# Kernel tuning notes

Measured on AMD Instinct MI355X. Metric: run time of the kernel, lower is better.

Reference implementation:

```python
import jax, jax.numpy as jnp
import numpy as np

N_HEADS = 4

def setup_inputs() -> dict:
    key = jax.random.key(0)
    B, S, D = 4, 2048, 256
    ks = jax.random.split(key, 9)
    sd = 1.0 / np.sqrt(D)
    return {
        "x":  jax.random.normal(ks[0], (B, S, D), jnp.float32),
        "Wq": jax.random.normal(ks[1], (D, D), jnp.float32) * sd,
        "bq": jax.random.normal(ks[2], (D,), jnp.float32) * 0.02,
        "Wk": jax.random.normal(ks[3], (D, D), jnp.float32) * sd,
        "bk": jax.random.normal(ks[4], (D,), jnp.float32) * 0.02,
        "Wv": jax.random.normal(ks[5], (D, D), jnp.float32) * sd,
        "bv": jax.random.normal(ks[6], (D,), jnp.float32) * 0.02,
        "Wo": jax.random.normal(ks[7], (D, D), jnp.float32) * sd,
        "bo": jax.random.normal(ks[8], (D,), jnp.float32) * 0.02,
    }

def reference(x, Wq, bq, Wk, bk, Wv, bv, Wo, bo):
    B, S, D = x.shape
    H = N_HEADS
    W = D // H
    # QKV projections, split heads: (B,S,D) -> (B,H,S,W)
    def heads(t):
        return t.reshape(B, S, H, W).transpose(0, 2, 1, 3)
    q = heads(x @ Wq + bq)
    k = heads(x @ Wk + bk)
    v = heads(x @ Wv + bv)
    scores = jnp.einsum('bhqw,bhkw->bhqk', q, k) / jnp.sqrt(jnp.float32(W))
    # multiplicative distance-decay mask: mask[i,j] = (S - |i-j|)/S
    i = jnp.arange(S, dtype=jnp.float32)
    mask = (S - jnp.abs(i[:, None] - i[None, :])) / S  # (S,S)
    scores = jax.nn.softmax(scores * mask, axis=-1)
    h = jnp.einsum('bhqk,bhkw->bhqw', scores, v)
    h = h.transpose(0, 2, 1, 3).reshape(B, S, D)  # merge heads
    return h @ Wo + bo
```

## Files before the change

### kernel.cpp

```cpp
#include <hip/hip_runtime.h>
#include <hip/hip_bf16.h>

#define S_LEN 2048
#define DMODEL 256
#define NH 4
#define HDIM 64

typedef __attribute__((ext_vector_type(8))) short short8;
typedef __attribute__((ext_vector_type(4))) float floatx4;
typedef __hip_bfloat16 bf16;

__device__ __forceinline__ floatx4 mfma16(short8 a, short8 b, floatx4 c) {
    return __builtin_amdgcn_mfma_f32_16x16x32_bf16(a, b, c, 0, 0, 0);
}
__device__ __forceinline__ void gload16(const void* gp, void* lp) {
    __builtin_amdgcn_global_load_lds(
        (const __attribute__((address_space(1))) void*)gp,
        (__attribute__((address_space(3))) void*)lp, 16, 0, 0);
}
__device__ __forceinline__ unsigned cvtpk(float lo, float hi) {
    unsigned r;
    asm("v_cvt_pk_bf16_f32 %0, %1, %2" : "=v"(r) : "v"(lo), "v"(hi));
    return r;
}
__device__ __forceinline__ void p32swap(int &a, int &b) {
    auto res = __builtin_amdgcn_permlane32_swap((unsigned)a, (unsigned)b, false, false);
    a = (int)res[0]; b = (int)res[1];
}
#if __has_builtin(__builtin_amdgcn_permlane16_swap)
#define HAVE_P16 1
__device__ __forceinline__ void p16swap(int &a, int &b) {
    auto res = __builtin_amdgcn_permlane16_swap((unsigned)a, (unsigned)b, false, false);
    a = (int)res[0]; b = (int)res[1];
}
#else
#define HAVE_P16 0
#endif
__device__ __forceinline__ float ex2(float x) {
#if __has_builtin(__builtin_amdgcn_exp2f)
    return __builtin_amdgcn_exp2f(x);
#else
    return __expf(x * 0.6931471805599453f);
#endif
}

__global__ __launch_bounds__(256) void prep_kernel(
    const float* __restrict__ x,
    const float* __restrict__ Wq, const float* __restrict__ Wk,
    const float* __restrict__ Wv, const float* __restrict__ Wo,
    bf16* __restrict__ xb, bf16* __restrict__ wtq, bf16* __restrict__ wtk,
    bf16* __restrict__ wtv, bf16* __restrict__ wto)
{
    __shared__ bf16 sT[64 * 72];
    const int t = threadIdx.x;
    const int blk = blockIdx.x;
    if (blk < 256) {
        int base = blk * 8192 + t * 8;
#pragma unroll
        for (int j = 0; j < 4; ++j) {
            int idx = base + j * 2048;
            float4 f0 = *(const float4*)&x[idx];
            float4 f1 = *(const float4*)&x[idx + 4];
            union { bf16 h[8]; short8 v; } o;
            o.h[0] = __float2bfloat16(f0.x); o.h[1] = __float2bfloat16(f0.y);
            o.h[2] = __float2bfloat16(f0.z); o.h[3] = __float2bfloat16(f0.w);
            o.h[4] = __float2bfloat16(f1.x); o.h[5] = __float2bfloat16(f1.y);
            o.h[6] = __float2bfloat16(f1.z); o.h[7] = __float2bfloat16(f1.w);
            *(short8*)&xb[idx] = o.v;
        }
    } else {
        int blk2 = blk - 256;
        int wi = blk2 >> 2;
        int n0 = (blk2 & 3) * 64;
        const float* ws = (wi == 0) ? Wq : (wi == 1) ? Wk : (wi == 2) ? Wv : Wo;
        bf16* wd = (wi == 0) ? wtq : (wi == 1) ? wtk : (wi == 2) ? wtv : wto;
        for (int k0 = 0; k0 < 256; k0 += 64) {
            __syncthreads();
#pragma unroll
            for (int j = 0; j < 16; ++j) {
                int idx = j * 256 + t;
                int kk = idx >> 6, nn = idx & 63;
                sT[nn * 72 + kk] = __float2bfloat16(ws[(k0 + kk) * 256 + n0 + nn]);
            }
            __syncthreads();
#pragma unroll
            for (int j2 = 0; j2 < 2; ++j2) {
                int c = j2 * 256 + t;
                int nn = c >> 3, seg = c & 7;
                *(short8*)&wd[(n0 + nn) * 256 + k0 + seg * 8] = *(const short8*)&sT[nn * 72 + seg * 8];
            }
        }
    }
}

__global__ __launch_bounds__(256) void proj_kernel(
    const bf16* __restrict__ xb, const bf16* __restrict__ hb,
    const bf16* __restrict__ wtq, const bf16* __restrict__ wtk,
    const bf16* __restrict__ wtv, const bf16* __restrict__ wto,
    const float* __restrict__ bq, const float* __restrict__ bk,
    const float* __restrict__ bvb, const float* __restrict__ bo,
    bf16* __restrict__ qo, bf16* __restrict__ ko, bf16* __restrict__ vt,
    float* __restrict__ oout, int mode_base)
{
    __shared__ __align__(16) char sm[65536];
    const int t = threadIdx.x, w = t >> 6, lane = t & 63;
    const int g = lane >> 4, r = lane & 15;
    const int mode = mode_base + blockIdx.z;
    const int bx = blockIdx.x, by = blockIdx.y;

    const char* Asrc; const char* Bsrc;
    if (mode == 0)      { Asrc = (const char*)(xb  + (size_t)bx * 64 * 256); Bsrc = (const char*)(wtq + (size_t)by * 64 * 256); }
    else if (mode == 1) { Asrc = (const char*)(xb  + (size_t)bx * 64 * 256); Bsrc = (const char*)(wtk + (size_t)by * 64 * 256); }
    else if (mode == 2) { Asrc = (const char*)(wtv + (size_t)by * 64 * 256); Bsrc = (const char*)(xb  + (size_t)bx * 64 * 256); }
    else                { Asrc = (const char*)(hb  + (size_t)bx * 64 * 256); Bsrc = (const char*)(wto + (size_t)by * 64 * 256); }

    const int row8 = t >> 5;
    const int w16 = t & 31;
#pragma unroll
    for (int c = 0; c < 8; ++c) {
        int row = c * 8 + row8;
        int sw = w16 ^ (row & 15);
        gload16(Asrc + row * 512 + sw * 16, sm + row * 512 + w16 * 16);
    }
#pragma unroll
    for (int c = 0; c < 8; ++c) {
        int row = c * 8 + row8;
        int sw = w16 ^ (row & 15);
        gload16(Bsrc + row * 512 + sw * 16, sm + 32768 + row * 512 + w16 * 16);
    }
    __syncthreads();

    const bf16* A = (const bf16*)sm;
    const bf16* B = (const bf16*)(sm + 32768);

    short8 af[8];
#pragma unroll
    for (int kf = 0; kf < 8; ++kf)
        af[kf] = *(const short8*)&A[(w * 16 + r) * 256 + (((kf * 4 + g) ^ r) * 8)];

    floatx4 acc[4];
#pragma unroll
    for (int nf = 0; nf < 4; ++nf) acc[nf] = (floatx4)0.f;
#pragma unroll
    for (int kf = 0; kf < 8; ++kf) {
#pragma unroll
        for (int nf = 0; nf < 4; ++nf) {
            short8 bfr = *(const short8*)&B[(nf * 16 + r) * 256 + (((kf * 4 + g) ^ r) * 8)];
            acc[nf] = mfma16(af[kf], bfr, acc[nf]);
        }
    }

    if (mode <= 1) {
        const float* bias = mode ? bk : bq;
        bf16* dst = mode ? ko : qo;
#pragma unroll
        for (int nf = 0; nf < 4; ++nf) {
            int n = by * 64 + nf * 16 + r;
            float bb = bias[n];
            int h = n >> 6, ww = n & 63;
#pragma unroll
            for (int i = 0; i < 4; ++i) {
                int m = bx * 64 + w * 16 + g * 4 + i;
                int b = m >> 11, s = m & 2047;
                dst[(((b * NH + h) * S_LEN) + s) * HDIM + ww] = __float2bfloat16(acc[nf][i] + bb);
            }
        }
    } else if (mode == 2) {
#pragma unroll
        for (int sf = 0; sf < 4; ++sf) {
#pragma unroll
            for (int i = 0; i < 4; ++i) {
                int feat = by * 64 + w * 16 + g * 4 + i;
                int scol = bx * 64 + sf * 16 + r;
                float v = acc[sf][i] + bvb[feat];
                int b = scol >> 11, s = scol & 2047;
                vt[((size_t)((b * NH + (feat >> 6)) * HDIM + (feat & 63))) * S_LEN + s] = __float2bfloat16(v);
            }
        }
    } else {
#pragma unroll
        for (int nf = 0; nf < 4; ++nf) {
            int n = by * 64 + nf * 16 + r;
            float bb = bo[n];
#pragma unroll
            for (int i = 0; i < 4; ++i) {
                int m = bx * 64 + w * 16 + g * 4 + i;
                oout[(size_t)m * 256 + n] = acc[nf][i] + bb;
            }
        }
    }
}

__global__ __launch_bounds__(512, 4) void attn_kernel(
    const bf16* __restrict__ q, const bf16* __restrict__ kmat,
    const bf16* __restrict__ vt, bf16* __restrict__ hout)
{
    __shared__ __align__(16) char smem[65536];
    const int t = threadIdx.x, wid = t >> 6, lane = t & 63;
    const int g = lane >> 4, r = lane & 15;
    const int qg = wid >> 1, hh = wid & 1;
    const int F = blockIdx.y * 32 + blockIdx.x;
    const int bh = ((F & 7) << 1) | ((F >> 3) & 1);
    const int q0 = (F >> 4) * 64;

    const bf16* srcp[4]; int ldsoff[4]; int sstride[4];
#pragma unroll
    for (int qi = 0; qi < 4; ++qi) {
        int idx = wid * 4 + qi;
        int arr = idx >> 3;
        int chunkbase = (idx & 7) * 64;
        int chunk = chunkbase + lane;
        int row = chunk >> 3, seg = chunk & 7, segx = seg ^ (row & 7);
        if (arr < 2) {
            srcp[qi] = kmat + ((size_t)(bh * S_LEN + arr * 1024 + row)) * HDIM + segx * 8;
            sstride[qi] = 64 * HDIM;
        } else {
            srcp[qi] = vt + ((size_t)(bh * HDIM + row)) * S_LEN + (arr - 2) * 1024 + segx * 8;
            sstride[qi] = 64;
        }
        ldsoff[qi] = arr * 8192 + chunkbase * 16;
    }

    const bf16* qb = q + ((size_t)(bh * S_LEN + q0 + qg * 16 + r)) * HDIM;
    short8 qf0 = *(const short8*)&qb[g * 8];
    short8 qf1 = *(const short8*)&qb[32 + g * 8];

    const int xk0 = ((0 + g) ^ (r & 7)) * 8 + r * 64;
    const int xk1 = ((4 + g) ^ (r & 7)) * 8 + r * 64;

    floatx4 oacc[4];
#pragma unroll
    for (int nf = 0; nf < 4; ++nf) oacc[nf] = (floatx4)0.f;
    float m_run = -1e30f, l_run = 0.f;

    const float iqf = (float)(q0 + qg * 16 + r);
    const float e0 = iqf - (float)(g * 4);
    const float C2  = 0.125f * 1.4426950408889634f;
    const float CN2 = 1.4426950408889634f / 16384.0f;

#pragma unroll
    for (int qi = 0; qi < 4; ++qi) { gload16(srcp[qi], smem + ldsoff[qi]); srcp[qi] += sstride[qi]; }
    __syncthreads();

    for (int it = 0; it < 16; ++it) {
        int buf = it & 1;
        if (it < 15) {
            char* nb = smem + (buf ^ 1) * 32768;
#pragma unroll
            for (int qi = 0; qi < 4; ++qi) { gload16(srcp[qi], nb + ldsoff[qi]); srcp[qi] += sstride[qi]; }
        }
        const bf16* sK = (const bf16*)(smem + buf * 32768 + hh * 8192);
        const bf16* sV = (const bf16*)(smem + buf * 32768 + 16384 + hh * 8192);

        floatx4 sc[4];
#pragma unroll
        for (int nt = 0; nt < 4; ++nt) sc[nt] = (floatx4)0.f;
        __builtin_amdgcn_s_setprio(1);
#pragma unroll
        for (int nt = 0; nt < 4; ++nt) {
            short8 kf0 = *(const short8*)&sK[nt * 1024 + xk0];
            short8 kf1 = *(const short8*)&sK[nt * 1024 + xk1];
            sc[nt] = mfma16(kf0, qf0, sc[nt]);
            sc[nt] = mfma16(kf1, qf1, sc[nt]);
        }
        __builtin_amdgcn_s_setprio(0);
        int kv0 = hh * 1024 + it * 64;
        float u_ = e0 - (float)kv0;
#pragma unroll
        for (int nt = 0; nt < 4; ++nt) {
            float tnt = u_ - (float)(nt * 16);
#pragma unroll
            for (int i = 0; i < 4; ++i) {
                float d = tnt - (float)i;
                float mmv = fmaf(fabsf(d), -CN2, C2);
                sc[nt][i] *= mmv;
            }
        }
        float vm = sc[0][0];
#pragma unroll
        for (int nt = 0; nt < 4; ++nt)
#pragma unroll
            for (int i = 0; i < 4; ++i) vm = fmaxf(vm, sc[nt][i]);
        vm = fmaxf(vm, __shfl_xor(vm, 16));
        vm = fmaxf(vm, __shfl_xor(vm, 32));
        if (!__all(vm <= m_run + 8.0f)) {
            float mn = fmaxf(m_run, vm);
            float c_ = ex2(m_run - mn);
            m_run = mn;
            l_run *= c_;
#pragma unroll
            for (int nf = 0; nf < 4; ++nf)
#pragma unroll
                for (int i = 0; i < 4; ++i) oacc[nf][i] *= c_;
        }
        float s0 = 0.f;
#pragma unroll
        for (int nt = 0; nt < 4; ++nt)
#pragma unroll
            for (int i = 0; i < 4; ++i) {
                float p = ex2(sc[nt][i] - m_run);
                sc[nt][i] = p;
                s0 += p;
            }
        s0 += __shfl_xor(s0, 16);
        s0 += __shfl_xor(s0, 32);
        l_run += s0;

        int wp[4][2];
#pragma unroll
        for (int nt = 0; nt < 4; ++nt) {
            wp[nt][0] = (int)cvtpk(sc[nt][0], sc[nt][1]);
            wp[nt][1] = (int)cvtpk(sc[nt][2], sc[nt][3]);
        }
        short8 pfrag[2];
#pragma unroll
        for (int kf = 0; kf < 2; ++kf) {
            int a0 = wp[2 * kf][0], a1 = wp[2 * kf][1];
            int b0 = wp[2 * kf + 1][0], b1 = wp[2 * kf + 1][1];
            p32swap(a0, b0);
            p32swap(a1, b1);
            union { int u[4]; short8 s; } pf;
#if HAVE_P16
            p16swap(a0, b0);
            p16swap(a1, b1);
            pf.u[0] = a0; pf.u[1] = a1; pf.u[2] = b0; pf.u[3] = b1;
#else
            const bool godd = (lane & 16) != 0;
            int sx0 = __shfl_xor(a0, 16);
            int sy0 = __shfl_xor(b0, 16);
            int sx1 = __shfl_xor(a1, 16);
            int sy1 = __shfl_xor(b1, 16);
            pf.u[0] = godd ? sy0 : a0;
            pf.u[1] = godd ? sy1 : a1;
            pf.u[2] = godd ? b0 : sx0;
            pf.u[3] = godd ? b1 : sx1;
#endif
            pfrag[kf] = pf.s;
        }
        __builtin_amdgcn_s_setprio(1);
#pragma unroll
        for (int nf = 0; nf < 4; ++nf) {
            short8 vf0 = *(const short8*)&sV[nf * 1024 + xk0];
            short8 vf1 = *(const short8*)&sV[nf * 1024 + xk1];
            oacc[nf] = mfma16(vf0, pfrag[0], oacc[nf]);
            oacc[nf] = mfma16(vf1, pfrag[1], oacc[nf]);
        }
        __builtin_amdgcn_s_setprio(0);
        __syncthreads();
    }

    float* sO = (float*)smem;
    float* sml = (float*)(smem + 16896);
    if (hh == 1) {
#pragma unroll
        for (int nf = 0; nf < 4; ++nf)
#pragma unroll
            for (int i = 0; i < 4; ++i)
                sO[(qg * 16 + r) * 66 + nf * 16 + g * 4 + i] = oacc[nf][i];
        if (g == 0) {
            sml[(qg * 16 + r) * 2 + 0] = m_run;
            sml[(qg * 16 + r) * 2 + 1] = l_run;
        }
    }
    __syncthreads();
    if (hh == 0) {
        float pm = sml[(qg * 16 + r) * 2 + 0];
        float pl = sml[(qg * 16 + r) * 2 + 1];
        float M = fmaxf(m_run, pm);
        float c0 = ex2(m_run - M), c1 = ex2(pm - M);
        float rec = 1.f / (c0 * l_run + c1 * pl);
        int b = bh >> 2, hd = bh & 3;
        int srow = q0 + qg * 16 + r;
        bf16* outp = hout + ((size_t)(b * S_LEN + srow)) * DMODEL + hd * HDIM;
#pragma unroll
        for (int nf = 0; nf < 4; ++nf) {
            union { bf16 h[4]; unsigned long long u; } ov;
#pragma unroll
            for (int i = 0; i < 4; ++i) {
                float po = sO[(qg * 16 + r) * 66 + nf * 16 + g * 4 + i];
                ov.h[i] = __float2bfloat16((c0 * oacc[nf][i] + c1 * po) * rec);
            }
            *(unsigned long long*)&outp[nf * 16 + g * 4] = ov.u;
        }
    }
}

extern "C" void kernel_launch(void* const* d_in, const int* in_sizes, int n_in,
                              void* d_out, int out_size, void* d_ws, size_t ws_size,
                              hipStream_t stream) {
    const float* x  = (const float*)d_in[0];
    const float* Wq = (const float*)d_in[1];
    const float* bq = (const float*)d_in[2];
    const float* Wk = (const float*)d_in[3];
    const float* bk = (const float*)d_in[4];
    const float* Wv = (const float*)d_in[5];
    const float* bv = (const float*)d_in[6];
    const float* Wo = (const float*)d_in[7];
    const float* bo = (const float*)d_in[8];

    char* ws = (char*)d_ws;
    bf16* xb  = (bf16*)(ws + 0);
    bf16* wtq = (bf16*)(ws + 4194304);
    bf16* wtk = (bf16*)(ws + 4325376);
    bf16* wtv = (bf16*)(ws + 4456448);
    bf16* wto = (bf16*)(ws + 4587520);
    bf16* qws = (bf16*)(ws + 4718592);
    bf16* kws = (bf16*)(ws + 8912896);
    bf16* vtw = (bf16*)(ws + 13107200);
    bf16* hws = (bf16*)(ws + 17301504);

    prep_kernel<<<272, 256, 0, stream>>>(x, Wq, Wk, Wv, Wo, xb, wtq, wtk, wtv, wto);
    proj_kernel<<<dim3(128, 4, 3), 256, 0, stream>>>(xb, hws, wtq, wtk, wtv, wto,
                                                     bq, bk, bv, bo, qws, kws, vtw,
                                                     (float*)d_out, 0);
    attn_kernel<<<dim3(32, 16), 512, 0, stream>>>(qws, kws, vtw, hws);
    proj_kernel<<<dim3(128, 4, 1), 256, 0, stream>>>(xb, hws, wtq, wtk, wtv, wto,
                                                     bq, bk, bv, bo, qws, kws, vtw,
                                                     (float*)d_out, 3);
}
```

Baseline: 129.5 us.

## Split weight transpose across more blocks, use fine-grained waitcnt barriers and tree reductions

The weight-transpose part of prep_kernel now gives each 64x64 tile its own block, with 320 blocks launched instead of 272, so the serial k0 loop and its extra barriers are gone. In the attention loop, the __syncthreads calls become explicit s_waitcnt vmcnt plus s_barrier. This lets the prefetch of the next K/V buffer stay in flight while waiting only on the current one. The row max and sum reductions now use balanced trees and a permlane32 swap in place of a shfl_xor across 32 lanes. The hand-written waitcnt relies on the global_load_lds count being exactly 4 per iteration, and a wrong count would make the kernel silently incorrect.

```diff
diff --git a/kernel.cpp b/kernel.cpp
--- a/kernel.cpp
+++ b/kernel.cpp
@@ -42,6 +42,16 @@
 #else
     return __expf(x * 0.6931471805599453f);
 #endif
+}
+__device__ __forceinline__ float xmax32(float x) {
+    int v = __float_as_int(x), w = v;
+    p32swap(v, w);
+    return fmaxf(__int_as_float(v), __int_as_float(w));
+}
+__device__ __forceinline__ float xsum32(float x) {
+    int v = __float_as_int(x), w = v;
+    p32swap(v, w);
+    return __int_as_float(v) + __int_as_float(w);
 }
 
 __global__ __launch_bounds__(256) void prep_kernel(
@@ -70,25 +80,23 @@
         }
     } else {
         int blk2 = blk - 256;
-        int wi = blk2 >> 2;
-        int n0 = (blk2 & 3) * 64;
-        const float* ws = (wi == 0) ? Wq : (wi == 1) ? Wk : (wi == 2) ? Wv : Wo;
+        int wi = blk2 >> 4;
+        int rem = blk2 & 15;
+        int n0 = (rem >> 2) * 64, k0 = (rem & 3) * 64;
+        const float* wsrc = (wi == 0) ? Wq : (wi == 1) ? Wk : (wi == 2) ? Wv : Wo;
         bf16* wd = (wi == 0) ? wtq : (wi == 1) ? wtk : (wi == 2) ? wtv : wto;
-        for (int k0 = 0; k0 < 256; k0 += 64) {
-            __syncthreads();
-#pragma unroll
-            for (int j = 0; j < 16; ++j) {
-                int idx = j * 256 + t;
-                int kk = idx >> 6, nn = idx & 63;
-                sT[nn * 72 + kk] = __float2bfloat16(ws[(k0 + kk) * 256 + n0 + nn]);
-            }
-            __syncthreads();
-#pragma unroll
-            for (int j2 = 0; j2 < 2; ++j2) {
-                int c = j2 * 256 + t;
-                int nn = c >> 3, seg = c & 7;
-                *(short8*)&wd[(n0 + nn) * 256 + k0 + seg * 8] = *(const short8*)&sT[nn * 72 + seg * 8];
-            }
+#pragma unroll
+        for (int j = 0; j < 16; ++j) {
+            int idx = j * 256 + t;
+            int kk = idx >> 6, nn = idx & 63;
+            sT[nn * 72 + kk] = __float2bfloat16(wsrc[(k0 + kk) * 256 + n0 + nn]);
+        }
+        __syncthreads();
+#pragma unroll
+        for (int j2 = 0; j2 < 2; ++j2) {
+            int c = j2 * 256 + t;
+            int nn = c >> 3, seg = c & 7;
+            *(short8*)&wd[(n0 + nn) * 256 + k0 + seg * 8] = *(const short8*)&sT[nn * 72 + seg * 8];
         }
     }
 }
@@ -240,7 +248,6 @@
 
 #pragma unroll
     for (int qi = 0; qi < 4; ++qi) { gload16(srcp[qi], smem + ldsoff[qi]); srcp[qi] += sstride[qi]; }
-    __syncthreads();
 
     for (int it = 0; it < 16; ++it) {
         int buf = it & 1;
@@ -248,7 +255,12 @@
             char* nb = smem + (buf ^ 1) * 32768;
 #pragma unroll
             for (int qi = 0; qi < 4; ++qi) { gload16(srcp[qi], nb + ldsoff[qi]); srcp[qi] += sstride[qi]; }
-        }
+            asm volatile("s_waitcnt vmcnt(4)" ::: "memory");
+        } else {
+            asm volatile("s_waitcnt vmcnt(0)" ::: "memory");
+        }
+        asm volatile("s_barrier" ::: "memory");
+
         const bf16* sK = (const bf16*)(smem + buf * 32768 + hh * 8192);
         const bf16* sV = (const bf16*)(smem + buf * 32768 + 16384 + hh * 8192);
 
@@ -276,13 +288,13 @@
                 sc[nt][i] *= mmv;
             }
         }
-        float vm = sc[0][0];
-#pragma unroll
-        for (int nt = 0; nt < 4; ++nt)
-#pragma unroll
-            for (int i = 0; i < 4; ++i) vm = fmaxf(vm, sc[nt][i]);
+        float m0a = fmaxf(fmaxf(sc[0][0], sc[0][1]), fmaxf(sc[0][2], sc[0][3]));
+        float m1a = fmaxf(fmaxf(sc[1][0], sc[1][1]), fmaxf(sc[1][2], sc[1][3]));
+        float m2a = fmaxf(fmaxf(sc[2][0], sc[2][1]), fmaxf(sc[2][2], sc[2][3]));
+        float m3a = fmaxf(fmaxf(sc[3][0], sc[3][1]), fmaxf(sc[3][2], sc[3][3]));
+        float vm = fmaxf(fmaxf(m0a, m1a), fmaxf(m2a, m3a));
         vm = fmaxf(vm, __shfl_xor(vm, 16));
-        vm = fmaxf(vm, __shfl_xor(vm, 32));
+        vm = xmax32(vm);
         if (!__all(vm <= m_run + 8.0f)) {
             float mn = fmaxf(m_run, vm);
             float c_ = ex2(m_run - mn);
@@ -293,17 +305,17 @@
 #pragma unroll
                 for (int i = 0; i < 4; ++i) oacc[nf][i] *= c_;
         }
-        float s0 = 0.f;
 #pragma unroll
         for (int nt = 0; nt < 4; ++nt)
 #pragma unroll
-            for (int i = 0; i < 4; ++i) {
-                float p = ex2(sc[nt][i] - m_run);
-                sc[nt][i] = p;
-                s0 += p;
-            }
+            for (int i = 0; i < 4; ++i) sc[nt][i] = ex2(sc[nt][i] - m_run);
+        float s0a = (sc[0][0] + sc[0][1]) + (sc[0][2] + sc[0][3]);
+        float s1a = (sc[1][0] + sc[1][1]) + (sc[1][2] + sc[1][3]);
+        float s2a = (sc[2][0] + sc[2][1]) + (sc[2][2] + sc[2][3]);
+        float s3a = (sc[3][0] + sc[3][1]) + (sc[3][2] + sc[3][3]);
+        float s0 = (s0a + s1a) + (s2a + s3a);
         s0 += __shfl_xor(s0, 16);
-        s0 += __shfl_xor(s0, 32);
+        s0 = xsum32(s0);
         l_run += s0;
 
         int wp[4][2];
@@ -346,7 +358,7 @@
             oacc[nf] = mfma16(vf1, pfrag[1], oacc[nf]);
         }
         __builtin_amdgcn_s_setprio(0);
-        __syncthreads();
+        asm volatile("s_barrier" ::: "memory");
     }
 
     float* sO = (float*)smem;
@@ -409,7 +421,7 @@
     bf16* vtw = (bf16*)(ws + 13107200);
     bf16* hws = (bf16*)(ws + 17301504);
 
-    prep_kernel<<<272, 256, 0, stream>>>(x, Wq, Wk, Wv, Wo, xb, wtq, wtk, wtv, wto);
+    prep_kernel<<<320, 256, 0, stream>>>(x, Wq, Wk, Wv, Wo, xb, wtq, wtk, wtv, wto);
     proj_kernel<<<dim3(128, 4, 3), 256, 0, stream>>>(xb, hws, wtq, wtk, wtv, wto,
                                                      bq, bk, bv, bo, qws, kws, vtw,
                                                      (float*)d_out, 0);
```

New measurement: 127.9 us. No clear change (-1.2%).
